# Performance work log

Hardware: AMD Instinct MI355X
Metric: run time of the kernel (lower is better)

The kernel has to match this reference:

```python
import jax, jax.numpy as jnp
import numpy as np
from jax import lax


def _conv1x1(x, w, b=None):
    # x: [N,C,H,W], w: [O,C]
    y = jnp.einsum('nchw,oc->nohw', x, w)
    if b is not None:
        y = y + b[None, :, None, None]
    return y


def _bn(x, g, b, rm, rv):
    # eval-mode BatchNorm2d, eps=1e-5 (torch default)
    inv = g / jnp.sqrt(rv + 1e-5)
    return x * inv[None, :, None, None] + (b - rm * inv)[None, :, None, None]


def setup_inputs() -> dict:
    key = jax.random.key(0)
    ks = jax.random.split(key, 32)
    N, C1, C2, H, W = 16, 256, 256, 64, 64
    mid = C2 // 16  # local_att reduction=16
    f32 = jnp.float32
    def nrm(k, shp, s=0.05):
        return s * jax.random.normal(k, shp, f32)
    return dict(
        x1=jax.random.normal(ks[0], (N, C1, H, W), f32),
        x2=jax.random.normal(ks[1], (N, C2, H, W), f32),
        conv1_w=nrm(ks[2], (C2, C1)), conv1_b=nrm(ks[3], (C2,)),
        conv2_w=nrm(ks[4], (C2, C2)), conv2_b=nrm(ks[5], (C2,)),
        conv3_w=nrm(ks[6], (C2, C2)), conv3_b=nrm(ks[7], (C2,)),
        conv4_w=nrm(ks[8], (C2, C2)), conv4_b=nrm(ks[9], (C2,)),
        conv4g_w=nrm(ks[10], (1, C2)), conv4g_b=nrm(ks[11], (1,)),
        bn_g=1.0 + nrm(ks[12], (C2,)), bn_b=nrm(ks[13], (C2,)),
        bn_rm=nrm(ks[14], (C2,)), bn_rv=1.0 + 0.1 * jax.random.uniform(ks[15], (C2,), f32),
        gamma=jax.random.normal(ks[16], (C2, 1, 1), f32), beta=jnp.zeros((C2, 1, 1), f32),
        gate_w=nrm(ks[17], (C2, C2)), gate_b=nrm(ks[18], (C2,)),
        dw_w=nrm(ks[19], (C2, 1, 3, 3)), dw_b=nrm(ks[20], (C2,)),
        interact_w=nrm(ks[21], (C2 // 4, C2 // 4)), interact_b=0.5 + nrm(ks[22], (C2 // 4,)),
        ca_w=nrm(ks[23], (1, 1, 5)),  # channel_att conv1d kernel, k=5 for C=256
        la1_w=nrm(ks[24], (mid, C2)),
        la_bn_g=1.0 + nrm(ks[25], (mid,)), la_bn_b=nrm(ks[26], (mid,)),
        la_bn_rm=nrm(ks[27], (mid,)), la_bn_rv=1.0 + 0.1 * jax.random.uniform(ks[28], (mid,), f32),
        fh_w=nrm(ks[29], (C2, mid)), fw_w=nrm(ks[30], (C2, mid)),
    )


def reference(x1, x2, conv1_w, conv1_b, conv2_w, conv2_b, conv3_w, conv3_b,
              conv4_w, conv4_b, conv4g_w, conv4g_b, bn_g, bn_b, bn_rm, bn_rv,
              gamma, beta, gate_w, gate_b, dw_w, dw_b, interact_w, interact_b,
              ca_w, la1_w, la_bn_g, la_bn_b, la_bn_rm, la_bn_rv, fh_w, fw_w):
    N, _, H, W = x1.shape
    C = conv1_w.shape[0]
    g1 = _conv1x1(x1, conv1_w, conv1_b)
    w1 = jax.nn.sigmoid(_bn(g1, bn_g, bn_b, bn_rm, bn_rv))
    g2 = _conv1x1(x2, conv2_w, conv2_b)
    w2 = jax.nn.sigmoid(_bn(g2, bn_g, bn_b, bn_rm, bn_rv))
    XG = g1 + g2

    # channel_att: GAP -> conv1d(k=5) across channels -> sigmoid gate
    y = XG.mean((2, 3))[:, None, :]  # [N,1,C]
    y = lax.conv_general_dilated(y, ca_w, (1,), [(2, 2)],
                                 dimension_numbers=('NCH', 'OIH', 'NCH'))
    temp = XG * jax.nn.sigmoid(y[:, 0, :])[:, :, None, None]

    # spatial sigmoid gate then 4-way group interact + softmax reweight
    Xs = jax.nn.sigmoid(_conv1x1(XG, conv4g_w, conv4g_b)) * XG
    C4 = C // 4
    Xr = Xs.reshape(N, 4, C4, H, W)
    o1 = jnp.einsum('ngchw,oc->ngohw', Xr, interact_w) + interact_b[None, None, :, None, None]
    xmap = o1.reshape(N, 4, 1, C4 * H * W)
    xav = xmap / xmap.mean(-1, keepdims=True)
    soft = jax.nn.softmax(xav, axis=2)  # softmax over size-1 dim -> ones (faithful)
    out = (soft.reshape(N, 4, C4, H, W) * Xr).reshape(N, C, H, W)

    # per-group (16) normalization using X_GOBAL stats (std unbiased, ddof=1)
    GN = 16
    xs = XG.reshape(N, GN, -1)
    mu = xs.mean(-1, keepdims=True)
    sd = jnp.std(xs, axis=-1, keepdims=True, ddof=1)
    x_gui = ((out.reshape(N, GN, -1) - mu) / (sd + 1e-10)).reshape(N, C, H, W)
    x_gui = x_gui * gamma[None] + beta[None]

    # threshold masks vs global-avg sigmoid reweights
    rw = jax.nn.sigmoid(XG.mean((2, 3), keepdims=True))  # [N,C,1,1]
    up1 = rw >= w1
    up2 = rw >= w2
    zero = jnp.zeros((), XG.dtype)
    x_up = jnp.where(up1, XG, zero) + jnp.where(up2, XG, zero)
    x_low = jnp.where(~up1, XG, zero) + jnp.where(~up2, XG, zero)

    # low branch: dwconv3x3 -> 1x1 -> channel-softmax gate
    dw = lax.conv_general_dilated(x_low, dw_w, (1, 1), [(1, 1), (1, 1)],
                                  dimension_numbers=('NCHW', 'OIHW', 'NCHW'),
                                  feature_group_count=C) + dw_b[None, :, None, None]
    x11 = _conv1x1(dw, conv3_w, conv3_b)
    gate = jax.nn.softmax(jax.nn.relu(x_low.mean((2, 3)) @ gate_w.T + gate_b), axis=1)
    xL = x11 * gate[:, :, None, None] + _conv1x1(x_up, conv4_w, conv4_b) + x_gui + temp

    # local_att (coordinate attention)
    xh = jnp.swapaxes(xL.mean(3, keepdims=True), 2, 3)  # [N,C,1,H]
    xw = xL.mean(2, keepdims=True)                       # [N,C,1,W]
    yc = jax.nn.relu(_bn(_conv1x1(jnp.concatenate([xh, xw], 3), la1_w),
                         la_bn_g, la_bn_b, la_bn_rm, la_bn_rv))
    sh = jax.nn.sigmoid(_conv1x1(jnp.swapaxes(yc[..., :H], 2, 3), fh_w))  # [N,C,H,1]
    sw = jax.nn.sigmoid(_conv1x1(yc[..., H:], fw_w))                      # [N,C,1,W]
    return xL * sh * sw
```

## Files before the change

### kernel.cpp

```cpp
#include <hip/hip_runtime.h>
#include <cstddef>
#include <cstdint>

constexpr int NN = 16, CC = 256, HH = 64, WW = 64, HW = 64 * 64;
constexpr size_t FSZ = (size_t)NN * CC * HW;

typedef short bf16x8 __attribute__((ext_vector_type(8)));
typedef float f32x4 __attribute__((ext_vector_type(4)));

__device__ __forceinline__ float sigmoidf_(float x) { return 1.f / (1.f + expf(-x)); }

__device__ __forceinline__ unsigned short bf16_rne(float f) {
    uint32_t u = __builtin_bit_cast(uint32_t, f);
    u += 0x7FFFu + ((u >> 16) & 1u);
    return (unsigned short)(u >> 16);
}
__device__ __forceinline__ float bf16_tof(unsigned short h) {
    uint32_t u = ((uint32_t)h) << 16;
    return __builtin_bit_cast(float, u);
}

__device__ __forceinline__ void gload16(const void* g, void* l) {
    __builtin_amdgcn_global_load_lds((const __attribute__((address_space(1))) void*)g,
                                     (__attribute__((address_space(3))) void*)l, 16, 0, 0);
}


__global__ __launch_bounds__(256) void wsplit_kernel(
    const float* __restrict__ w1, const float* __restrict__ w2,
    const float* __restrict__ w3, const float* __restrict__ w4,
    unsigned short* __restrict__ w1h, unsigned short* __restrict__ w1m, unsigned short* __restrict__ w1l,
    unsigned short* __restrict__ w2h, unsigned short* __restrict__ w2m, unsigned short* __restrict__ w2l,
    unsigned short* __restrict__ w4h, unsigned short* __restrict__ w4l,
    unsigned short* __restrict__ w3b,
    float* __restrict__ zstat, float* __restrict__ zspix) {
    const int i = blockIdx.x * 256 + threadIdx.x;
    const int o = i >> 8, c = i & 255;
    const size_t fo = ((size_t)((o >> 4) * 8 + (c >> 5))) * 512 +
                      (size_t)(((c & 31) >> 3) * 128 + (o & 15) * 8 + (c & 7));
    {
        float x = w1[i];
        unsigned short h = bf16_rne(x); float r = x - bf16_tof(h);
        unsigned short m = bf16_rne(r); float r2 = r - bf16_tof(m);
        w1h[fo] = h; w1m[fo] = m; w1l[fo] = bf16_rne(r2);
    }
    {
        float x = w2[i];
        unsigned short h = bf16_rne(x); float r = x - bf16_tof(h);
        unsigned short m = bf16_rne(r); float r2 = r - bf16_tof(m);
        w2h[fo] = h; w2m[fo] = m; w2l[fo] = bf16_rne(r2);
    }
    {
        float x = w4[i];
        unsigned short h = bf16_rne(x); float r = x - bf16_tof(h);
        w4h[fo] = h; w4l[fo] = bf16_rne(r);
    }
    w3b[fo] = bf16_rne(w3[i]);
    if (i < 8192) zstat[i] = 0.f;
    zspix[i] = 0.f;
}

__global__ __launch_bounds__(256) void tsplit3_kernel(const float* __restrict__ X,
                                                      unsigned short* __restrict__ O0,
                                                      unsigned short* __restrict__ O1,
                                                      unsigned short* __restrict__ O2) {
    const int hw0 = blockIdx.x * 64, c0 = blockIdx.y * 64, n = blockIdx.z;
    __shared__ float sT[64][65];
    const int tid = threadIdx.x;
    {
        const int hwl = (tid & 15) << 2;
        const int cl = tid >> 4;
#pragma unroll
        for (int p = 0; p < 4; ++p) {
            const int c = cl + p * 16;
            const float4 v = *(const float4*)(X + ((size_t)(n * CC + c0 + c)) * HW + hw0 + hwl);
            sT[c][hwl] = v.x; sT[c][hwl + 1] = v.y; sT[c][hwl + 2] = v.z; sT[c][hwl + 3] = v.w;
        }
    }
    __syncthreads();
    const int hwl = tid >> 2, cb = (tid & 3) << 4;
    unsigned short h[16], m[16], l[16];
#pragma unroll
    for (int j = 0; j < 16; ++j) {
        const float x = sT[cb + j][hwl];
        const unsigned short hh = bf16_rne(x);
        h[j] = hh;
        const float r = x - bf16_tof(hh);
        const unsigned short mm = bf16_rne(r);
        m[j] = mm;
        l[j] = bf16_rne(r - bf16_tof(mm));
    }
    const size_t ob = ((size_t)(n * HW + hw0 + hwl)) * 256 + c0 + cb;
    *(int4*)(O0 + ob) = *(int4*)&h[0]; *(int4*)(O0 + ob + 8) = *(int4*)&h[8];
    *(int4*)(O1 + ob) = *(int4*)&m[0]; *(int4*)(O1 + ob + 8) = *(int4*)&m[8];
    *(int4*)(O2 + ob) = *(int4*)&l[0]; *(int4*)(O2 + ob + 8) = *(int4*)&l[8];
}

__global__ __launch_bounds__(256) void tsplit_bf16_kernel(const unsigned short* __restrict__ X,
                                                          unsigned short* __restrict__ O0) {
    const int hw0 = blockIdx.x * 64, c0 = blockIdx.y * 64, n = blockIdx.z;
    __shared__ unsigned short sT[64][72];
    const int tid = threadIdx.x;
    {
        const int cl = tid >> 3;
        const int ch = (tid & 7) * 8;
#pragma unroll
        for (int p = 0; p < 2; ++p) {
            const int c = cl + p * 32;
            const int4 v = *(const int4*)(X + ((size_t)(n * CC + c0 + c)) * HW + hw0 + ch);
            *(int4*)&sT[c][ch] = v;
        }
    }
    __syncthreads();
    const int hwl = tid >> 2, cb = (tid & 3) << 4;
    unsigned short h[16];
#pragma unroll
    for (int j = 0; j < 16; ++j) h[j] = sT[cb + j][hwl];
    const size_t ob = ((size_t)(n * HW + hw0 + hwl)) * 256 + c0 + cb;
    *(int4*)(O0 + ob) = *(int4*)&h[0]; *(int4*)(O0 + ob + 8) = *(int4*)&h[8];
}

template <int NS>
__device__ __forceinline__ void mfma_core6(const unsigned short* __restrict__ X0,
                                           const unsigned short* __restrict__ X1,
                                           const unsigned short* __restrict__ X2,
                                           const unsigned short* __restrict__ W0,
                                           const unsigned short* __restrict__ W1,
                                           const unsigned short* __restrict__ W2,
                                           int n, int hw0, int o0, f32x4 (&acc)[2][4]) {
    __shared__ unsigned short sX[2][NS][64][32];
    const int tid = threadIdx.x;
    const int lane = tid & 63, wv = tid >> 6, quad = lane >> 4, nlo = lane & 15;
    const int srow = tid >> 2;
    const int schunk = (tid & 3) ^ ((srow >> 1) & 3);
    const unsigned short* Xs[3] = {X0, X1, X2};
    const unsigned short* Ws[3] = {W0, W1, W2};
    const size_t xg = ((size_t)(n * HW + hw0 + srow)) * 256 + schunk * 8;
    const unsigned short* wp[NS];
#pragma unroll
    for (int s = 0; s < NS; ++s)
        wp[s] = Ws[s] + ((size_t)((o0 >> 4) + wv) * 8) * 512 + (size_t)lane * 8;

    int roff[4];
#pragma unroll
    for (int nt = 0; nt < 4; ++nt) {
        const int rrow = nt * 16 + nlo;
        roff[nt] = rrow * 32 + (quad ^ ((rrow >> 1) & 3)) * 8;
    }

    bf16x8 af[2][NS][2];
#pragma unroll
    for (int s = 0; s < NS; ++s)
        gload16(Xs[s] + xg, &sX[0][s][wv * 16][0]);
#pragma unroll
    for (int s = 0; s < NS; ++s)
#pragma unroll
        for (int f = 0; f < 2; ++f)
            af[0][s][f] = *(const bf16x8*)(wp[s] + ((size_t)(f * 32)) * 512);
    __syncthreads();

#pragma unroll
    for (int ks = 0; ks < 8; ++ks) {
        const int cur = ks & 1;
        if (ks < 7) {
#pragma unroll
            for (int s = 0; s < NS; ++s)
                gload16(Xs[s] + xg + (ks + 1) * 32, &sX[cur ^ 1][s][wv * 16][0]);
#pragma unroll
            for (int s = 0; s < NS; ++s)
#pragma unroll
                for (int f = 0; f < 2; ++f)
                    af[cur ^ 1][s][f] = *(const bf16x8*)(wp[s] + ((size_t)(f * 32 + ks + 1)) * 512);
        }
#pragma unroll
        for (int nt = 0; nt < 4; ++nt) {
            bf16x8 bfr[NS];
#pragma unroll
            for (int s = 0; s < NS; ++s)
                bfr[s] = *(const bf16x8*)&sX[cur][s][0][roff[nt]];
#pragma unroll
            for (int f = 0; f < 2; ++f) {
                if (NS == 3) {
                    acc[f][nt] = __builtin_amdgcn_mfma_f32_16x16x32_bf16(af[cur][1][f], bfr[1], acc[f][nt], 0, 0, 0);
                    acc[f][nt] = __builtin_amdgcn_mfma_f32_16x16x32_bf16(af[cur][0][f], bfr[2], acc[f][nt], 0, 0, 0);
                    acc[f][nt] = __builtin_amdgcn_mfma_f32_16x16x32_bf16(af[cur][2][f], bfr[0], acc[f][nt], 0, 0, 0);
                    acc[f][nt] = __builtin_amdgcn_mfma_f32_16x16x32_bf16(af[cur][0][f], bfr[1], acc[f][nt], 0, 0, 0);
                    acc[f][nt] = __builtin_amdgcn_mfma_f32_16x16x32_bf16(af[cur][1][f], bfr[0], acc[f][nt], 0, 0, 0);
                    acc[f][nt] = __builtin_amdgcn_mfma_f32_16x16x32_bf16(af[cur][0][f], bfr[0], acc[f][nt], 0, 0, 0);
                } else if (NS == 2) {
                    acc[f][nt] = __builtin_amdgcn_mfma_f32_16x16x32_bf16(af[cur][0][f], bfr[1], acc[f][nt], 0, 0, 0);
                    acc[f][nt] = __builtin_amdgcn_mfma_f32_16x16x32_bf16(af[cur][1][f], bfr[0], acc[f][nt], 0, 0, 0);
                    acc[f][nt] = __builtin_amdgcn_mfma_f32_16x16x32_bf16(af[cur][0][f], bfr[0], acc[f][nt], 0, 0, 0);
                } else {
                    acc[f][nt] = __builtin_amdgcn_mfma_f32_16x16x32_bf16(af[cur][0][f], bfr[0], acc[f][nt], 0, 0, 0);
                }
            }
        }
        __syncthreads();
    }
}

__device__ __forceinline__ void mfma_core_pair(const unsigned short* __restrict__ XUH,
                                               const unsigned short* __restrict__ XUL,
                                               const unsigned short* __restrict__ XDW,
                                               const unsigned short* __restrict__ W4H,
                                               const unsigned short* __restrict__ W4L,
                                               const unsigned short* __restrict__ W3B,
                                               int n, int hw0, int o0,
                                               f32x4 (&acc_a)[2][4], f32x4 (&acc_b)[2][4]) {
    __shared__ unsigned short sX[2][3][64][32];
    const int tid = threadIdx.x;
    const int lane = tid & 63, wv = tid >> 6, quad = lane >> 4, nlo = lane & 15;
    const int srow = tid >> 2;
    const int schunk = (tid & 3) ^ ((srow >> 1) & 3);
    const unsigned short* Xs[3] = {XUH, XUL, XDW};
    const unsigned short* Ws[3] = {W4H, W4L, W3B};
    const size_t xg = ((size_t)(n * HW + hw0 + srow)) * 256 + schunk * 8;
    const unsigned short* wp[3];
#pragma unroll
    for (int s = 0; s < 3; ++s)
        wp[s] = Ws[s] + ((size_t)((o0 >> 4) + wv) * 8) * 512 + (size_t)lane * 8;

    int roff[4];
#pragma unroll
    for (int nt = 0; nt < 4; ++nt) {
        const int rrow = nt * 16 + nlo;
        roff[nt] = rrow * 32 + (quad ^ ((rrow >> 1) & 3)) * 8;
    }

    bf16x8 af[2][3][2];
#pragma unroll
    for (int s = 0; s < 3; ++s)
        gload16(Xs[s] + xg, &sX[0][s][wv * 16][0]);
#pragma unroll
    for (int s = 0; s < 3; ++s)
#pragma unroll
        for (int f = 0; f < 2; ++f)
            af[0][s][f] = *(const bf16x8*)(wp[s] + ((size_t)(f * 32)) * 512);
    __syncthreads();

#pragma unroll
    for (int ks = 0; ks < 8; ++ks) {
        const int cur = ks & 1;
        if (ks < 7) {
#pragma unroll
            for (int s = 0; s < 3; ++s)
                gload16(Xs[s] + xg + (ks + 1) * 32, &sX[cur ^ 1][s][wv * 16][0]);
#pragma unroll
            for (int s = 0; s < 3; ++s)
#pragma unroll
                for (int f = 0; f < 2; ++f)
                    af[cur ^ 1][s][f] = *(const bf16x8*)(wp[s] + ((size_t)(f * 32 + ks + 1)) * 512);
        }
#pragma unroll
        for (int nt = 0; nt < 4; ++nt) {
            bf16x8 bfr[3];
#pragma unroll
            for (int s = 0; s < 3; ++s)
                bfr[s] = *(const bf16x8*)&sX[cur][s][0][roff[nt]];
#pragma unroll
            for (int f = 0; f < 2; ++f) {
                acc_a[f][nt] = __builtin_amdgcn_mfma_f32_16x16x32_bf16(af[cur][0][f], bfr[1], acc_a[f][nt], 0, 0, 0);
                acc_a[f][nt] = __builtin_amdgcn_mfma_f32_16x16x32_bf16(af[cur][1][f], bfr[0], acc_a[f][nt], 0, 0, 0);
                acc_a[f][nt] = __builtin_amdgcn_mfma_f32_16x16x32_bf16(af[cur][0][f], bfr[0], acc_a[f][nt], 0, 0, 0);
                acc_b[f][nt] = __builtin_amdgcn_mfma_f32_16x16x32_bf16(af[cur][2][f], bfr[2], acc_b[f][nt], 0, 0, 0);
            }
        }
        __syncthreads();
    }
}

template <int NS>
__global__ __launch_bounds__(256, 3) void gemm_mfma_kernel(
    const unsigned short* __restrict__ X0, const unsigned short* __restrict__ X1,
    const unsigned short* __restrict__ X2, const unsigned short* __restrict__ W0,
    const unsigned short* __restrict__ W1, const unsigned short* __restrict__ W2,
    const float* __restrict__ bias, float* __restrict__ Y) {
    const int hw0 = blockIdx.x * 64, o0 = blockIdx.y * 128, n = blockIdx.z;
    f32x4 acc[2][4] = {};
    mfma_core6<NS>(X0, X1, X2, W0, W1, W2, n, hw0, o0, acc);
    const int lane = threadIdx.x & 63, wv = threadIdx.x >> 6;
    const int quad = lane >> 4, nlo = lane & 15;
#pragma unroll
    for (int f = 0; f < 2; ++f) {
        const int om = o0 + f * 64 + wv * 16 + quad * 4;
#pragma unroll
        for (int nt = 0; nt < 4; ++nt) {
            const int hw = hw0 + nt * 16 + nlo;
#pragma unroll
            for (int r = 0; r < 4; ++r) {
                const int o = om + r;
                Y[((size_t)(n * CC + o)) * HW + hw] = acc[f][nt][r] + bias[o];
            }
        }
    }
}

__global__ __launch_bounds__(256, 3) void gemm_xg_kernel(
    const unsigned short* __restrict__ X0, const unsigned short* __restrict__ X1,
    const unsigned short* __restrict__ X2, const unsigned short* __restrict__ W0,
    const unsigned short* __restrict__ W1, const unsigned short* __restrict__ W2,
    const float* __restrict__ bias, const float* __restrict__ g1,
    const float* __restrict__ cgw,
    float* __restrict__ XG, float* __restrict__ sum_c, float* __restrict__ sq_c,
    float* __restrict__ s_pix) {
    const int hw0 = blockIdx.x * 64, o0 = blockIdx.y * 128, n = blockIdx.z;
    f32x4 acc[2][4] = {};
    mfma_core6<3>(X0, X1, X2, W0, W1, W2, n, hw0, o0, acc);
    __shared__ float sRed[4][64];
    const int lane = threadIdx.x & 63, wv = threadIdx.x >> 6;
    const int quad = lane >> 4, nlo = lane & 15;
    float pnt[4] = {0.f, 0.f, 0.f, 0.f};
#pragma unroll
    for (int f = 0; f < 2; ++f) {
        const int om = o0 + f * 64 + wv * 16 + quad * 4;
#pragma unroll
        for (int r = 0; r < 4; ++r) {
            const int o = om + r;
            const float b = bias[o];
            const float wg = cgw[o];
            float s = 0.f, q = 0.f;
#pragma unroll
            for (int nt = 0; nt < 4; ++nt) {
                const int hw = hw0 + nt * 16 + nlo;
                const size_t rowi = ((size_t)(n * CC + o)) * HW + hw;
                const float xgv = acc[f][nt][r] + b + g1[rowi];
                XG[rowi] = xgv;
                s += xgv; q += xgv * xgv;
                pnt[nt] += wg * xgv;
            }
#pragma unroll
            for (int off = 1; off < 16; off <<= 1) { s += __shfl_xor(s, off); q += __shfl_xor(q, off); }
            if (nlo == 0) { atomicAdd(&sum_c[n * CC + o], s); atomicAdd(&sq_c[n * CC + o], q); }
        }
    }
#pragma unroll
    for (int nt = 0; nt < 4; ++nt) {
        float p = pnt[nt];
        p += __shfl_xor(p, 16); p += __shfl_xor(p, 32);
        if (quad == 0) sRed[wv][nt * 16 + nlo] = p;
    }
    __syncthreads();
    if (threadIdx.x < 64) {
        const float s2 = sRed[0][threadIdx.x] + sRed[1][threadIdx.x] +
                         sRed[2][threadIdx.x] + sRed[3][threadIdx.x];
        atomicAdd(&s_pix[n * HW + hw0 + threadIdx.x], s2);
    }
}

__global__ __launch_bounds__(256, 3) void gemm_final_kernel(
    const unsigned short* __restrict__ XUH, const unsigned short* __restrict__ XUL,
    const unsigned short* __restrict__ XDW,
    const unsigned short* __restrict__ W4H, const unsigned short* __restrict__ W4L,
    const unsigned short* __restrict__ W3B,
    const float* __restrict__ b3, const float* __restrict__ b4,
    const float* __restrict__ XG, const float* __restrict__ s_pix,
    const float* __restrict__ cgb,
    const float* __restrict__ gate, const float* __restrict__ ca_sig,
    const float* __restrict__ mu_g, const float* __restrict__ isd_g,
    const float* __restrict__ gamma, const float* __restrict__ beta,
    float* __restrict__ out) {
    const int hw0 = blockIdx.x * 64, o0 = blockIdx.y * 128, n = blockIdx.z;
    f32x4 acc_a[2][4] = {};
    f32x4 acc_b[2][4] = {};
    mfma_core_pair(XUH, XUL, XDW, W4H, W4L, W3B, n, hw0, o0, acc_a, acc_b);
    const int lane = threadIdx.x & 63, wv = threadIdx.x >> 6;
    const int quad = lane >> 4, nlo = lane & 15;
    const float cgb0 = cgb[0];
#pragma unroll
    for (int f = 0; f < 2; ++f) {
        const int om = o0 + f * 64 + wv * 16 + quad * 4;
#pragma unroll
        for (int nt = 0; nt < 4; ++nt) {
            const int hw = hw0 + nt * 16 + nlo;
            const int pix = n * HW + hw;
            const float sp = sigmoidf_(s_pix[pix] + cgb0);
#pragma unroll
            for (int r = 0; r < 4; ++r) {
                const int o = om + r;
                const float g = gate[n * CC + o];
                const float cs = ca_sig[n * CC + o];
                const float mu = mu_g[n * 16 + (o >> 4)];
                const float isd = isd_g[n * 16 + (o >> 4)];
                const size_t rowi = ((size_t)(n * CC + o)) * HW + hw;
                const float xg = XG[rowi];
                const float gui = (sp * xg - mu) * isd * gamma[o] + beta[o];
                out[rowi] = (acc_b[f][nt][r] + b3[o]) * g + (acc_a[f][nt][r] + b4[o]) + gui + xg * cs;
            }
        }
    }
}

__global__ __launch_bounds__(256) void stats2_kernel(const float* __restrict__ sum_c,
                                                     const float* __restrict__ sq_c,
                                                     const float* __restrict__ caw,
                                                     float* __restrict__ rw,
                                                     float* __restrict__ ca_sig,
                                                     float* __restrict__ mu_g,
                                                     float* __restrict__ isd_g,
                                                     float* __restrict__ xlow_sum) {
    const int n = blockIdx.x, c = threadIdx.x;
    __shared__ float m[256];
    const float mean = sum_c[n * CC + c] * (1.f / (float)HW);
    m[c] = mean;
    rw[n * CC + c] = sigmoidf_(mean);
    xlow_sum[n * CC + c] = 0.f;
    __syncthreads();
    float y = 0.f;
#pragma unroll
    for (int k = 0; k < 5; ++k) {
        const int cc = c - 2 + k;
        if (cc >= 0 && cc < 256) y += m[cc] * caw[k];
    }
    ca_sig[n * CC + c] = sigmoidf_(y);
    if (c < 16) {
        float S = 0.f, Q = 0.f;
        for (int j = 0; j < 16; ++j) {
            S += sum_c[n * CC + c * 16 + j];
            Q += sq_c[n * CC + c * 16 + j];
        }
        const float cnt = 65536.f;
        const float mu = S / cnt;
        float var = (Q - S * S / cnt) * (1.f / (cnt - 1.f));
        var = fmaxf(var, 0.f);
        mu_g[n * 16 + c] = mu;
        isd_g[n * 16 + c] = 1.f / (sqrtf(var) + 1e-10f);
    }
}

__global__ __launch_bounds__(256) void masks_split_kernel(
    float* g1_xlow,
    const float* __restrict__ XG,
    const float* __restrict__ rw,
    const float* __restrict__ bng, const float* __restrict__ bnb,
    const float* __restrict__ bnrm, const float* __restrict__ bnrv,
    unsigned short* __restrict__ O0, unsigned short* __restrict__ O1,
    float* __restrict__ xlow_sum) {
    const int hw0 = blockIdx.x * 64, c0 = blockIdx.y * 64, n = blockIdx.z;
    __shared__ float sT[64][65];
    const int tid = threadIdx.x;
    const int cl = tid >> 2;
    const int q = tid & 3;
    const int c = c0 + cl;
    const float inv = bng[c] / sqrtf(bnrv[c] + 1e-5f);
    const float off = bnb[c] - bnrm[c] * inv;
    const float rwv = rw[n * CC + c];
    const size_t rowb = ((size_t)(n * CC + c)) * HW + hw0;
    float lsum = 0.f;
#pragma unroll
    for (int j = 0; j < 4; ++j) {
        const int hwl = q * 4 + j * 16;
        const float4 a = *(const float4*)(g1_xlow + rowb + hwl);
        const float4 x = *(const float4*)(XG + rowb + hwl);
        const float* ap = &a.x; const float* xp = &x.x;
        float4 xlv;
        float* xlp = &xlv.x;
#pragma unroll
        for (int e = 0; e < 4; ++e) {
            const float g2e = xp[e] - ap[e];
            const float w1 = sigmoidf_(inv * ap[e] + off);
            const float w2 = sigmoidf_(inv * g2e + off);
            const float cu = (rwv >= w1 ? 1.f : 0.f) + (rwv >= w2 ? 1.f : 0.f);
            const float xu = xp[e] * cu;
            const float xl = xp[e] * (2.f - cu);
            sT[cl][hwl + e] = xu;
            xlp[e] = xl;
            lsum += xl;
        }
        *(float4*)(g1_xlow + rowb + hwl) = xlv;
    }
    lsum += __shfl_xor(lsum, 1);
    lsum += __shfl_xor(lsum, 2);
    if (q == 0) atomicAdd(&xlow_sum[n * CC + c], lsum);
    __syncthreads();
    const int hwl2 = tid >> 2, cb = (tid & 3) << 4;
    unsigned short h[16], m[16];
#pragma unroll
    for (int j = 0; j < 16; ++j) {
        const float x = sT[cb + j][hwl2];
        const unsigned short hh = bf16_rne(x);
        h[j] = hh;
        m[j] = bf16_rne(x - bf16_tof(hh));
    }
    const size_t ob = ((size_t)(n * HW + hw0 + hwl2)) * 256 + c0 + cb;
    *(int4*)(O0 + ob) = *(int4*)&h[0]; *(int4*)(O0 + ob + 8) = *(int4*)&h[8];
    *(int4*)(O1 + ob) = *(int4*)&m[0]; *(int4*)(O1 + ob + 8) = *(int4*)&m[8];
}

__global__ __launch_bounds__(256) void gate_kernel(const float* __restrict__ xlow_sum,
                                                   const float* __restrict__ gatew,
                                                   const float* __restrict__ gateb,
                                                   float* __restrict__ gate) {
    const int n = blockIdx.x, c = threadIdx.x;
    __shared__ float xm[256];
    __shared__ float red[256];
    xm[c] = xlow_sum[n * CC + c] * (1.f / (float)HW);
    __syncthreads();
    float acc = gateb[c];
    const float* wr = gatew + (size_t)c * 256;
#pragma unroll 8
    for (int k = 0; k < 256; ++k) acc += xm[k] * wr[k];
    const float v = fmaxf(acc, 0.f);
    red[c] = v;
    __syncthreads();
    for (int s = 128; s > 0; s >>= 1) {
        if (c < s) red[c] = fmaxf(red[c], red[c + s]);
        __syncthreads();
    }
    const float mx = red[0];
    __syncthreads();
    const float e = expf(v - mx);
    red[c] = e;
    __syncthreads();
    for (int s = 128; s > 0; s >>= 1) {
        if (c < s) red[c] += red[c + s];
        __syncthreads();
    }
    gate[n * CC + c] = e / red[0];
}

__global__ __launch_bounds__(256) void dwconv_kernel(const float* __restrict__ xlow,
                                                     const float* __restrict__ dww,
                                                     const float* __restrict__ dwb,
                                                     unsigned short* __restrict__ out) {
    const int c = blockIdx.x & 255;
    __shared__ float sl[64][65];
    const size_t base = (size_t)blockIdx.x * HW;
    for (int r = 0; r < 16; ++r) {
        const int idx = threadIdx.x + r * 256;
        sl[idx >> 6][idx & 63] = xlow[base + idx];
    }
    float wk[9];
#pragma unroll
    for (int j = 0; j < 9; ++j) wk[j] = dww[c * 9 + j];
    const float bias = dwb[c];
    __syncthreads();
    for (int r = 0; r < 16; ++r) {
        const int idx = threadIdx.x + r * 256;
        const int h = idx >> 6, w = idx & 63;
        float acc = bias;
#pragma unroll
        for (int dh = 0; dh < 3; ++dh) {
            const int hh = h + dh - 1;
            if (hh < 0 || hh > 63) continue;
#pragma unroll
            for (int dw2 = 0; dw2 < 3; ++dw2) {
                const int ww2 = w + dw2 - 1;
                if (ww2 < 0 || ww2 > 63) continue;
                acc += sl[hh][ww2] * wk[dh * 3 + dw2];
            }
        }
        out[base + idx] = bf16_rne(acc);
    }
}

__global__ __launch_bounds__(256) void pool_kernel(const float* __restrict__ xL,
                                                   float* __restrict__ xh,
                                                   float* __restrict__ xw) {
    __shared__ float sl[64][65];
    const size_t base = (size_t)blockIdx.x * HW;
    for (int r = 0; r < 16; ++r) {
        const int idx = threadIdx.x + r * 256;
        sl[idx >> 6][idx & 63] = xL[base + idx];
    }
    __syncthreads();
    const int t = threadIdx.x;
    if (t < 64) {
        float s = 0.f;
        for (int w = 0; w < 64; ++w) s += sl[t][w];
        xh[(size_t)blockIdx.x * 64 + t] = s * (1.f / 64.f);
    } else if (t < 128) {
        const int w = t - 64;
        float s = 0.f;
        for (int h = 0; h < 64; ++h) s += sl[h][w];
        xw[(size_t)blockIdx.x * 64 + w] = s * (1.f / 64.f);
    }
}

__global__ __launch_bounds__(256) void local_att_kernel(const float* __restrict__ xh,
                                                        const float* __restrict__ xw,
                                                        const float* __restrict__ la1w,
                                                        const float* __restrict__ lag,
                                                        const float* __restrict__ lab,
                                                        const float* __restrict__ larm,
                                                        const float* __restrict__ larv,
                                                        const float* __restrict__ fhw,
                                                        const float* __restrict__ fww,
                                                        float* __restrict__ sh,
                                                        float* __restrict__ sw) {
    const int n = blockIdx.x;
    __shared__ float w1s[16 * 256];
    __shared__ float fhs[256 * 16];
    __shared__ float fws[256 * 16];
    __shared__ float ycs[16][128];
    for (int i = threadIdx.x; i < 4096; i += 256) {
        w1s[i] = la1w[i];
        fhs[i] = fhw[i];
        fws[i] = fww[i];
    }
    __syncthreads();
    for (int idx = threadIdx.x; idx < 2048; idx += 256) {
        const int m = idx >> 7, p = idx & 127;
        const float* vsrc = (p < 64) ? (xh + (size_t)n * CC * 64 + p)
                                     : (xw + (size_t)n * CC * 64 + (p - 64));
        float acc = 0.f;
#pragma unroll 8
        for (int c = 0; c < 256; ++c) acc += w1s[m * 256 + c] * vsrc[(size_t)c * 64];
        const float inv = lag[m] / sqrtf(larv[m] + 1e-5f);
        const float off = lab[m] - larm[m] * inv;
        ycs[m][p] = fmaxf(inv * acc + off, 0.f);
    }
    __syncthreads();
    for (int idx = threadIdx.x; idx < 16384; idx += 256) {
        const int c = idx >> 6, h = idx & 63;
        float a1 = 0.f, a2 = 0.f;
#pragma unroll
        for (int m = 0; m < 16; ++m) {
            a1 += fhs[c * 16 + m] * ycs[m][h];
            a2 += fws[c * 16 + m] * ycs[m][64 + h];
        }
        sh[(size_t)n * CC * 64 + idx] = sigmoidf_(a1);
        sw[(size_t)n * CC * 64 + idx] = sigmoidf_(a2);
    }
}

__global__ __launch_bounds__(256) void final_kernel(const float* __restrict__ xL,
                                                    const float* __restrict__ sh,
                                                    const float* __restrict__ sw,
                                                    float* __restrict__ out) {
    __shared__ float shs[64], sws[64];
    const int t = threadIdx.x;
    if (t < 64) shs[t] = sh[(size_t)blockIdx.x * 64 + t];
    else if (t < 128) sws[t - 64] = sw[(size_t)blockIdx.x * 64 + (t - 64)];
    __syncthreads();
    const size_t base = (size_t)blockIdx.x * HW;
#pragma unroll 4
    for (int r = 0; r < 16; ++r) {
        const int idx = t + r * 256;
        out[base + idx] = xL[base + idx] * shs[idx >> 6] * sws[idx & 63];
    }
}

extern "C" void kernel_launch(void* const* d_in, const int* in_sizes, int n_in,
                              void* d_out, int out_size, void* d_ws, size_t ws_size,
                              hipStream_t stream) {
    const float* x1 = (const float*)d_in[0];
    const float* x2 = (const float*)d_in[1];
    const float* c1w = (const float*)d_in[2];
    const float* c1b = (const float*)d_in[3];
    const float* c2w = (const float*)d_in[4];
    const float* c2b = (const float*)d_in[5];
    const float* c3w = (const float*)d_in[6];
    const float* c3b = (const float*)d_in[7];
    const float* c4w = (const float*)d_in[8];
    const float* c4b = (const float*)d_in[9];
    const float* cgw = (const float*)d_in[10];
    const float* cgb = (const float*)d_in[11];
    const float* bng = (const float*)d_in[12];
    const float* bnb = (const float*)d_in[13];
    const float* bnrm = (const float*)d_in[14];
    const float* bnrv = (const float*)d_in[15];
    const float* gamma = (const float*)d_in[16];
    const float* beta = (const float*)d_in[17];
    const float* gatew = (const float*)d_in[18];
    const float* gateb = (const float*)d_in[19];
    const float* dww = (const float*)d_in[20];
    const float* dwb = (const float*)d_in[21];
    const float* caw = (const float*)d_in[24];
    const float* la1w = (const float*)d_in[25];
    const float* lag = (const float*)d_in[26];
    const float* lab = (const float*)d_in[27];
    const float* larm = (const float*)d_in[28];
    const float* larv = (const float*)d_in[29];
    const float* fhw = (const float*)d_in[30];
    const float* fww = (const float*)d_in[31];

    float* ws = (float*)d_ws;
    float* buf0 = ws;
    float* buf1 = ws + FSZ;
    float* buf2 = ws + 2 * FSZ;
    float* sp = ws + 3 * FSZ;
    float* sum_c = sp;    sp += 4096;
    float* sq_c = sp;     sp += 4096;
    float* rw = sp;       sp += 4096;
    float* ca_sig = sp;   sp += 4096;
    float* xlow_sum = sp; sp += 4096;
    float* mu_g = sp;     sp += 256;
    float* isd_g = sp;    sp += 256;
    float* s_pix = sp;    sp += (size_t)NN * HW;
    float* xh = sp;       sp += (size_t)NN * CC * 64;
    float* xwb = sp;      sp += (size_t)NN * CC * 64;
    float* shb = sp;      sp += (size_t)NN * CC * 64;
    float* swb = sp;      sp += (size_t)NN * CC * 64;
    unsigned short* wsp = (unsigned short*)shb;
    unsigned short* w1h = wsp + 0 * 65536;
    unsigned short* w1m = wsp + 1 * 65536;
    unsigned short* w1l = wsp + 2 * 65536;
    unsigned short* w2h = wsp + 3 * 65536;
    unsigned short* w2m = wsp + 4 * 65536;
    unsigned short* w2l = wsp + 5 * 65536;
    unsigned short* w4h = wsp + 6 * 65536;
    unsigned short* w4l = wsp + 7 * 65536;
    unsigned short* w3b = wsp + 8 * 65536;

    float* out = (float*)d_out;

    const dim3 gt(HW / 64, CC / 64, NN);
    const dim3 gg(HW / 64, CC / 128, NN);

    wsplit_kernel<<<256, 256, 0, stream>>>(c1w, c2w, c3w, c4w, w1h, w1m, w1l,
                                           w2h, w2m, w2l, w4h, w4l, w3b,
                                           sum_c, s_pix);
    {
        unsigned short* sx0 = (unsigned short*)buf1;
        unsigned short* sx1 = (unsigned short*)buf1 + FSZ;
        unsigned short* sx2 = (unsigned short*)buf2;
        tsplit3_kernel<<<gt, 256, 0, stream>>>(x1, sx0, sx1, sx2);
        gemm_mfma_kernel<3><<<gg, 256, 0, stream>>>(sx0, sx1, sx2, w1h, w1m, w1l, c1b, buf0);
    }
    {
        unsigned short* sx0 = (unsigned short*)out;
        unsigned short* sx1 = (unsigned short*)out + FSZ;
        unsigned short* sx2 = (unsigned short*)buf2;
        tsplit3_kernel<<<gt, 256, 0, stream>>>(x2, sx0, sx1, sx2);
        gemm_xg_kernel<<<gg, 256, 0, stream>>>(sx0, sx1, sx2, w2h, w2m, w2l, c2b,
                                               buf0, cgw, buf1, sum_c, sq_c, s_pix);
    }
    stats2_kernel<<<NN, 256, 0, stream>>>(sum_c, sq_c, caw, rw, ca_sig, mu_g, isd_g, xlow_sum);
    {
        unsigned short* ux0 = (unsigned short*)out;
        unsigned short* ux1 = (unsigned short*)out + FSZ;
        masks_split_kernel<<<gt, 256, 0, stream>>>(buf0, buf1, rw, bng, bnb, bnrm, bnrv,
                                                   ux0, ux1, xlow_sum);
    }
    float* gate = sum_c;
    gate_kernel<<<NN, 256, 0, stream>>>(xlow_sum, gatew, gateb, gate);
    dwconv_kernel<<<NN * CC, 256, 0, stream>>>(buf0, dww, dwb, (unsigned short*)buf2);
    tsplit_bf16_kernel<<<gt, 256, 0, stream>>>((const unsigned short*)buf2,
                                               (unsigned short*)buf0);
    {
        unsigned short* ux0 = (unsigned short*)out;
        unsigned short* ux1 = (unsigned short*)out + FSZ;
        unsigned short* sx0 = (unsigned short*)buf0;
        gemm_final_kernel<<<gg, 256, 0, stream>>>(ux0, ux1, sx0, w4h, w4l, w3b,
                                                  c3b, c4b, buf1, s_pix, cgb,
                                                  gate, ca_sig, mu_g, isd_g, gamma, beta,
                                                  buf2);
    }
    pool_kernel<<<NN * CC, 256, 0, stream>>>(buf2, xh, xwb);
    local_att_kernel<<<NN, 256, 0, stream>>>(xh, xwb, la1w, lag, lab, larm, larv,
                                             fhw, fww, shb, swb);
    final_kernel<<<NN * CC, 256, 0, stream>>>(buf2, shb, swb, out);
}
```

Before: 637.6 us.

## Triple-buffer LDS tiles with explicit vmcnt waits in MFMA GEMM cores

Switches the shared-memory X tiles in the three MFMA GEMM cores from double to triple buffering. Loads are issued two k-steps ahead, and the per-step __syncthreads is replaced by a partial s_waitcnt vmcnt plus a raw s_barrier, so global-to-LDS loads can overlap compute across more than one step. The aim is to hide global load latency in the GEMMs. It raises LDS use per block (which may reduce occupancy) and depends on hand-counted vmcnt values being correct.

Result: no change. 634.2 us (-0.5%).

```diff
diff --git a/kernel.cpp b/kernel.cpp
--- a/kernel.cpp
+++ b/kernel.cpp
@@ -120,15 +120,14 @@
     *(int4*)(O0 + ob) = *(int4*)&h[0]; *(int4*)(O0 + ob + 8) = *(int4*)&h[8];
 }
 
-template <int NS>
-__device__ __forceinline__ void mfma_core6(const unsigned short* __restrict__ X0,
+__device__ __forceinline__ void mfma_core8(const unsigned short* __restrict__ X0,
                                            const unsigned short* __restrict__ X1,
                                            const unsigned short* __restrict__ X2,
                                            const unsigned short* __restrict__ W0,
                                            const unsigned short* __restrict__ W1,
                                            const unsigned short* __restrict__ W2,
                                            int n, int hw0, int o0, f32x4 (&acc)[2][4]) {
-    __shared__ unsigned short sX[2][NS][64][32];
+    __shared__ unsigned short sX[3][3][64][32];
     const int tid = threadIdx.x;
     const int lane = tid & 63, wv = tid >> 6, quad = lane >> 4, nlo = lane & 15;
     const int srow = tid >> 2;
@@ -136,9 +135,9 @@
     const unsigned short* Xs[3] = {X0, X1, X2};
     const unsigned short* Ws[3] = {W0, W1, W2};
     const size_t xg = ((size_t)(n * HW + hw0 + srow)) * 256 + schunk * 8;
-    const unsigned short* wp[NS];
-#pragma unroll
-    for (int s = 0; s < NS; ++s)
+    const unsigned short* wp[3];
+#pragma unroll
+    for (int s = 0; s < 3; ++s)
         wp[s] = Ws[s] + ((size_t)((o0 >> 4) + wv) * 8) * 512 + (size_t)lane * 8;
 
     int roff[4];
@@ -148,67 +147,75 @@
         roff[nt] = rrow * 32 + (quad ^ ((rrow >> 1) & 3)) * 8;
     }
 
-    bf16x8 af[2][NS][2];
-#pragma unroll
-    for (int s = 0; s < NS; ++s)
+    bf16x8 af[2][3][2];
+#pragma unroll
+    for (int s = 0; s < 3; ++s)
         gload16(Xs[s] + xg, &sX[0][s][wv * 16][0]);
 #pragma unroll
-    for (int s = 0; s < NS; ++s)
+    for (int s = 0; s < 3; ++s)
 #pragma unroll
         for (int f = 0; f < 2; ++f)
             af[0][s][f] = *(const bf16x8*)(wp[s] + ((size_t)(f * 32)) * 512);
-    __syncthreads();
+#pragma unroll
+    for (int s = 0; s < 3; ++s)
+        gload16(Xs[s] + xg + 32, &sX[1][s][wv * 16][0]);
+    asm volatile("s_waitcnt vmcnt(9)" ::: "memory");
+    __builtin_amdgcn_s_barrier();
+    __builtin_amdgcn_sched_barrier(0);
 
 #pragma unroll
     for (int ks = 0; ks < 8; ++ks) {
-        const int cur = ks & 1;
+        const int cur = ks % 3;
+        const int c2 = ks & 1;
         if (ks < 7) {
 #pragma unroll
-            for (int s = 0; s < NS; ++s)
-                gload16(Xs[s] + xg + (ks + 1) * 32, &sX[cur ^ 1][s][wv * 16][0]);
-#pragma unroll
-            for (int s = 0; s < NS; ++s)
+            for (int s = 0; s < 3; ++s)
 #pragma unroll
                 for (int f = 0; f < 2; ++f)
-                    af[cur ^ 1][s][f] = *(const bf16x8*)(wp[s] + ((size_t)(f * 32 + ks + 1)) * 512);
+                    af[c2 ^ 1][s][f] = *(const bf16x8*)(wp[s] + ((size_t)(f * 32 + ks + 1)) * 512);
+        }
+        if (ks < 6) {
+#pragma unroll
+            for (int s = 0; s < 3; ++s)
+                gload16(Xs[s] + xg + (ks + 2) * 32, &sX[(ks + 2) % 3][s][wv * 16][0]);
         }
 #pragma unroll
         for (int nt = 0; nt < 4; ++nt) {
-            bf16x8 bfr[NS];
-#pragma unroll
-            for (int s = 0; s < NS; ++s)
+            bf16x8 bfr[3];
+#pragma unroll
+            for (int s = 0; s < 3; ++s)
                 bfr[s] = *(const bf16x8*)&sX[cur][s][0][roff[nt]];
 #pragma unroll
             for (int f = 0; f < 2; ++f) {
-                if (NS == 3) {
-                    acc[f][nt] = __builtin_amdgcn_mfma_f32_16x16x32_bf16(af[cur][1][f], bfr[1], acc[f][nt], 0, 0, 0);
-                    acc[f][nt] = __builtin_amdgcn_mfma_f32_16x16x32_bf16(af[cur][0][f], bfr[2], acc[f][nt], 0, 0, 0);
-                    acc[f][nt] = __builtin_amdgcn_mfma_f32_16x16x32_bf16(af[cur][2][f], bfr[0], acc[f][nt], 0, 0, 0);
-                    acc[f][nt] = __builtin_amdgcn_mfma_f32_16x16x32_bf16(af[cur][0][f], bfr[1], acc[f][nt], 0, 0, 0);
-                    acc[f][nt] = __builtin_amdgcn_mfma_f32_16x16x32_bf16(af[cur][1][f], bfr[0], acc[f][nt], 0, 0, 0);
-                    acc[f][nt] = __builtin_amdgcn_mfma_f32_16x16x32_bf16(af[cur][0][f], bfr[0], acc[f][nt], 0, 0, 0);
-                } else if (NS == 2) {
-                    acc[f][nt] = __builtin_amdgcn_mfma_f32_16x16x32_bf16(af[cur][0][f], bfr[1], acc[f][nt], 0, 0, 0);
-                    acc[f][nt] = __builtin_amdgcn_mfma_f32_16x16x32_bf16(af[cur][1][f], bfr[0], acc[f][nt], 0, 0, 0);
-                    acc[f][nt] = __builtin_amdgcn_mfma_f32_16x16x32_bf16(af[cur][0][f], bfr[0], acc[f][nt], 0, 0, 0);
-                } else {
-                    acc[f][nt] = __builtin_amdgcn_mfma_f32_16x16x32_bf16(af[cur][0][f], bfr[0], acc[f][nt], 0, 0, 0);
-                }
+                acc[f][nt] = __builtin_amdgcn_mfma_f32_16x16x32_bf16(af[c2][1][f], bfr[1], acc[f][nt], 0, 0, 0);
+                acc[f][nt] = __builtin_amdgcn_mfma_f32_16x16x32_bf16(af[c2][0][f], bfr[2], acc[f][nt], 0, 0, 0);
+                acc[f][nt] = __builtin_amdgcn_mfma_f32_16x16x32_bf16(af[c2][2][f], bfr[0], acc[f][nt], 0, 0, 0);
+                acc[f][nt] = __builtin_amdgcn_mfma_f32_16x16x32_bf16(af[c2][0][f], bfr[1], acc[f][nt], 0, 0, 0);
+                acc[f][nt] = __builtin_amdgcn_mfma_f32_16x16x32_bf16(af[c2][1][f], bfr[0], acc[f][nt], 0, 0, 0);
+                acc[f][nt] = __builtin_amdgcn_mfma_f32_16x16x32_bf16(af[c2][0][f], bfr[0], acc[f][nt], 0, 0, 0);
             }
         }
-        __syncthreads();
-    }
-}
-
-__device__ __forceinline__ void mfma_core_pair(const unsigned short* __restrict__ XUH,
-                                               const unsigned short* __restrict__ XUL,
-                                               const unsigned short* __restrict__ XDW,
-                                               const unsigned short* __restrict__ W4H,
-                                               const unsigned short* __restrict__ W4L,
-                                               const unsigned short* __restrict__ W3B,
-                                               int n, int hw0, int o0,
-                                               f32x4 (&acc_a)[2][4], f32x4 (&acc_b)[2][4]) {
-    __shared__ unsigned short sX[2][3][64][32];
+        if (ks < 6) {
+            asm volatile("s_waitcnt vmcnt(3)" ::: "memory");
+            __builtin_amdgcn_s_barrier();
+            __builtin_amdgcn_sched_barrier(0);
+        } else if (ks == 6) {
+            asm volatile("s_waitcnt vmcnt(6)" ::: "memory");
+            __builtin_amdgcn_s_barrier();
+            __builtin_amdgcn_sched_barrier(0);
+        }
+    }
+}
+
+__device__ __forceinline__ void mfma_core_pair8(const unsigned short* __restrict__ XUH,
+                                                const unsigned short* __restrict__ XUL,
+                                                const unsigned short* __restrict__ XDW,
+                                                const unsigned short* __restrict__ W4H,
+                                                const unsigned short* __restrict__ W4L,
+                                                const unsigned short* __restrict__ W3B,
+                                                int n, int hw0, int o0,
+                                                f32x4 (&acc_a)[2][4], f32x4 (&acc_b)[2][4]) {
+    __shared__ unsigned short sX[3][3][64][32];
     const int tid = threadIdx.x;
     const int lane = tid & 63, wv = tid >> 6, quad = lane >> 4, nlo = lane & 15;
     const int srow = tid >> 2;
@@ -237,20 +244,28 @@
 #pragma unroll
         for (int f = 0; f < 2; ++f)
             af[0][s][f] = *(const bf16x8*)(wp[s] + ((size_t)(f * 32)) * 512);
-    __syncthreads();
+#pragma unroll
+    for (int s = 0; s < 3; ++s)
+        gload16(Xs[s] + xg + 32, &sX[1][s][wv * 16][0]);
+    asm volatile("s_waitcnt vmcnt(9)" ::: "memory");
+    __builtin_amdgcn_s_barrier();
+    __builtin_amdgcn_sched_barrier(0);
 
 #pragma unroll
     for (int ks = 0; ks < 8; ++ks) {
-        const int cur = ks & 1;
+        const int cur = ks % 3;
+        const int c2 = ks & 1;
         if (ks < 7) {
 #pragma unroll
             for (int s = 0; s < 3; ++s)
-                gload16(Xs[s] + xg + (ks + 1) * 32, &sX[cur ^ 1][s][wv * 16][0]);
+#pragma unroll
+                for (int f = 0; f < 2; ++f)
+                    af[c2 ^ 1][s][f] = *(const bf16x8*)(wp[s] + ((size_t)(f * 32 + ks + 1)) * 512);
+        }
+        if (ks < 6) {
 #pragma unroll
             for (int s = 0; s < 3; ++s)
-#pragma unroll
-                for (int f = 0; f < 2; ++f)
-                    af[cur ^ 1][s][f] = *(const bf16x8*)(wp[s] + ((size_t)(f * 32 + ks + 1)) * 512);
+                gload16(Xs[s] + xg + (ks + 2) * 32, &sX[(ks + 2) % 3][s][wv * 16][0]);
         }
 #pragma unroll
         for (int nt = 0; nt < 4; ++nt) {
@@ -260,17 +275,24 @@
                 bfr[s] = *(const bf16x8*)&sX[cur][s][0][roff[nt]];
 #pragma unroll
             for (int f = 0; f < 2; ++f) {
-                acc_a[f][nt] = __builtin_amdgcn_mfma_f32_16x16x32_bf16(af[cur][0][f], bfr[1], acc_a[f][nt], 0, 0, 0);
-                acc_a[f][nt] = __builtin_amdgcn_mfma_f32_16x16x32_bf16(af[cur][1][f], bfr[0], acc_a[f][nt], 0, 0, 0);
-                acc_a[f][nt] = __builtin_amdgcn_mfma_f32_16x16x32_bf16(af[cur][0][f], bfr[0], acc_a[f][nt], 0, 0, 0);
-                acc_b[f][nt] = __builtin_amdgcn_mfma_f32_16x16x32_bf16(af[cur][2][f], bfr[2], acc_b[f][nt], 0, 0, 0);
+                acc_a[f][nt] = __builtin_amdgcn_mfma_f32_16x16x32_bf16(af[c2][0][f], bfr[1], acc_a[f][nt], 0, 0, 0);
+                acc_a[f][nt] = __builtin_amdgcn_mfma_f32_16x16x32_bf16(af[c2][1][f], bfr[0], acc_a[f][nt], 0, 0, 0);
+                acc_a[f][nt] = __builtin_amdgcn_mfma_f32_16x16x32_bf16(af[c2][0][f], bfr[0], acc_a[f][nt], 0, 0, 0);
+                acc_b[f][nt] = __builtin_amdgcn_mfma_f32_16x16x32_bf16(af[c2][2][f], bfr[2], acc_b[f][nt], 0, 0, 0);
             }
         }
-        __syncthreads();
-    }
-}
-
-template <int NS>
+        if (ks < 6) {
+            asm volatile("s_waitcnt vmcnt(3)" ::: "memory");
+            __builtin_amdgcn_s_barrier();
+            __builtin_amdgcn_sched_barrier(0);
+        } else if (ks == 6) {
+            asm volatile("s_waitcnt vmcnt(6)" ::: "memory");
+            __builtin_amdgcn_s_barrier();
+            __builtin_amdgcn_sched_barrier(0);
+        }
+    }
+}
+
 __global__ __launch_bounds__(256, 3) void gemm_mfma_kernel(
     const unsigned short* __restrict__ X0, const unsigned short* __restrict__ X1,
     const unsigned short* __restrict__ X2, const unsigned short* __restrict__ W0,
@@ -278,7 +300,7 @@
     const float* __restrict__ bias, float* __restrict__ Y) {
     const int hw0 = blockIdx.x * 64, o0 = blockIdx.y * 128, n = blockIdx.z;
     f32x4 acc[2][4] = {};
-    mfma_core6<NS>(X0, X1, X2, W0, W1, W2, n, hw0, o0, acc);
+    mfma_core8(X0, X1, X2, W0, W1, W2, n, hw0, o0, acc);
     const int lane = threadIdx.x & 63, wv = threadIdx.x >> 6;
     const int quad = lane >> 4, nlo = lane & 15;
 #pragma unroll
@@ -306,7 +328,7 @@
     float* __restrict__ s_pix) {
     const int hw0 = blockIdx.x * 64, o0 = blockIdx.y * 128, n = blockIdx.z;
     f32x4 acc[2][4] = {};
-    mfma_core6<3>(X0, X1, X2, W0, W1, W2, n, hw0, o0, acc);
+    mfma_core8(X0, X1, X2, W0, W1, W2, n, hw0, o0, acc);
     __shared__ float sRed[4][64];
     const int lane = threadIdx.x & 63, wv = threadIdx.x >> 6;
     const int quad = lane >> 4, nlo = lane & 15;
@@ -363,7 +385,7 @@
     const int hw0 = blockIdx.x * 64, o0 = blockIdx.y * 128, n = blockIdx.z;
     f32x4 acc_a[2][4] = {};
     f32x4 acc_b[2][4] = {};
-    mfma_core_pair(XUH, XUL, XDW, W4H, W4L, W3B, n, hw0, o0, acc_a, acc_b);
+    mfma_core_pair8(XUH, XUL, XDW, W4H, W4L, W3B, n, hw0, o0, acc_a, acc_b);
     const int lane = threadIdx.x & 63, wv = threadIdx.x >> 6;
     const int quad = lane >> 4, nlo = lane & 15;
     const float cgb0 = cgb[0];
@@ -716,7 +738,7 @@
         unsigned short* sx1 = (unsigned short*)buf1 + FSZ;
         unsigned short* sx2 = (unsigned short*)buf2;
         tsplit3_kernel<<<gt, 256, 0, stream>>>(x1, sx0, sx1, sx2);
-        gemm_mfma_kernel<3><<<gg, 256, 0, stream>>>(sx0, sx1, sx2, w1h, w1m, w1l, c1b, buf0);
+        gemm_mfma_kernel<<<gg, 256, 0, stream>>>(sx0, sx1, sx2, w1h, w1m, w1l, c1b, buf0);
     }
     {
         unsigned short* sx0 = (unsigned short*)out;
```
